# Kernel optimization log

Measured on AMD Instinct MI355X. Metric: run time of the kernel, lower is better.

The kernel has to match this reference:

```python
import jax, jax.numpy as jnp
import numpy as np

N, E, H, NODE_IN, EDGE_DIM, L = 10000, 400000, 128, 6, 3, 4
LN_EPS = 1e-5


def _lin_init(key, fan_in, fan_out):
    return jax.random.normal(key, (fan_in, fan_out), dtype=jnp.float32) / np.sqrt(fan_in)


def setup_inputs() -> dict:
    key = jax.random.key(0)
    ks = jax.random.split(key, 24)
    x = jax.random.normal(ks[0], (N, NODE_IN), dtype=jnp.float32)
    edge_index = jax.random.randint(ks[1], (2, E), 0, N, dtype=jnp.int64)
    edge_attr = jax.random.normal(ks[2], (E, EDGE_DIM), dtype=jnp.float32)
    # encoder
    enc_w1 = _lin_init(ks[3], NODE_IN, H); enc_b1 = jnp.zeros((H,), jnp.float32)
    enc_w2 = _lin_init(ks[4], H, H); enc_b2 = jnp.zeros((H,), jnp.float32)
    # per-layer stacked params [L, ...]
    msg_w1 = jax.vmap(lambda k: _lin_init(k, 2 * H + EDGE_DIM, H))(jax.random.split(ks[5], L))
    msg_b1 = jnp.zeros((L, H), jnp.float32)
    msg_w2 = jax.vmap(lambda k: _lin_init(k, H, H))(jax.random.split(ks[6], L))
    msg_b2 = jnp.zeros((L, H), jnp.float32)
    upd_w1 = jax.vmap(lambda k: _lin_init(k, 2 * H, H))(jax.random.split(ks[7], L))
    upd_b1 = jnp.zeros((L, H), jnp.float32)
    upd_w2 = jax.vmap(lambda k: _lin_init(k, H, H))(jax.random.split(ks[8], L))
    upd_b2 = jnp.zeros((L, H), jnp.float32)
    ln_g = jnp.ones((L, H), jnp.float32)
    ln_b = jnp.zeros((L, H), jnp.float32)
    # decoder
    dec_w1 = _lin_init(ks[9], H, H); dec_b1 = jnp.zeros((H,), jnp.float32)
    dec_w2 = _lin_init(ks[10], H, 1); dec_b2 = jnp.zeros((1,), jnp.float32)
    return dict(x=x, edge_index=edge_index, edge_attr=edge_attr,
                enc_w1=enc_w1, enc_b1=enc_b1, enc_w2=enc_w2, enc_b2=enc_b2,
                msg_w1=msg_w1, msg_b1=msg_b1, msg_w2=msg_w2, msg_b2=msg_b2,
                upd_w1=upd_w1, upd_b1=upd_b1, upd_w2=upd_w2, upd_b2=upd_b2,
                ln_g=ln_g, ln_b=ln_b,
                dec_w1=dec_w1, dec_b1=dec_b1, dec_w2=dec_w2, dec_b2=dec_b2)


def _layernorm(h, g, b):
    mu = jnp.mean(h, axis=-1, keepdims=True)
    var = jnp.mean(jnp.square(h - mu), axis=-1, keepdims=True)
    return (h - mu) * jax.lax.rsqrt(var + LN_EPS) * g + b


def reference(x, edge_index, edge_attr,
              enc_w1, enc_b1, enc_w2, enc_b2,
              msg_w1, msg_b1, msg_w2, msg_b2,
              upd_w1, upd_b1, upd_w2, upd_b2,
              ln_g, ln_b,
              dec_w1, dec_b1, dec_w2, dec_b2):
    src, tgt = edge_index[0], edge_index[1]  # PyG default flow: message from x_j=src to x_i=tgt
    # in-degree counts for mean aggregation (zero-degree nodes -> 0 output, like scatter_mean)
    counts = jax.ops.segment_sum(jnp.ones((E,), jnp.float32), tgt, num_segments=N)
    inv_counts = (1.0 / jnp.maximum(counts, 1.0))[:, None]
    # encoder
    h = jax.nn.relu(x @ enc_w1 + enc_b1) @ enc_w2 + enc_b2  # [N, H]
    for l in range(L):
        x_i = h[tgt]  # [E, H] target features
        x_j = h[src]  # [E, H] source features
        m_in = jnp.concatenate([x_i, x_j, edge_attr], axis=-1)  # [E, 2H+edge_dim]
        m = jax.nn.relu(m_in @ msg_w1[l] + msg_b1[l]) @ msg_w2[l] + msg_b2[l]  # [E, H]
        agg = jax.ops.segment_sum(m, tgt, num_segments=N) * inv_counts  # [N, H] mean aggregate
        u_in = jnp.concatenate([h, agg], axis=-1)  # [N, 2H]
        u = jax.nn.relu(u_in @ upd_w1[l] + upd_b1[l]) @ upd_w2[l] + upd_b2[l]
        h = _layernorm(u + h, ln_g[l], ln_b[l])  # residual (in==out channels)
    # decoder
    return jax.nn.relu(h @ dec_w1 + dec_b1) @ dec_w2 + dec_b2  # [N, 1]
```

## Files before the change

### kernel.cpp

```cpp
#include <hip/hip_runtime.h>

#define NN 10000
#define NE 400000
#define HD 128
#define NIN 6
#define EDIM 3
#define NL 4
#define CAP 96
#define LN_EPS 1e-5f

typedef unsigned short u16;
using short8 = __attribute__((ext_vector_type(8))) short;
using f32x4 = __attribute__((ext_vector_type(4))) float;

__device__ __forceinline__ u16 f2bf(float x) {
    unsigned u = __float_as_uint(x);
    return (u16)((u + 0x7fff + ((u >> 16) & 1)) >> 16);
}
__device__ __forceinline__ float bf2f(u16 h) { return __uint_as_float(((unsigned)h) << 16); }
__device__ __forceinline__ void split2(float x, u16& hi, u16& lo) {
    hi = f2bf(x);
    lo = f2bf(x - bf2f(hi));
}
#define MFMA(a, b, c) __builtin_amdgcn_mfma_f32_16x16x32_bf16((a), (b), (c), 0, 0, 0)


__global__ __launch_bounds__(256) void k_prep(const float* __restrict__ msg_w2, const float* __restrict__ msg_b2,
                                              const float* __restrict__ upd_w1, float* __restrict__ M2,
                                              float* __restrict__ c2, int* __restrict__ cnt) {
    int idx = blockIdx.x * 256 + threadIdx.x;
    if (idx < 65536) {
        int l = idx >> 14, rem = idx & 16383, i = rem >> 7, jj = rem & 127;
        const float* U1b = upd_w1 + (size_t)l * 2 * HD * HD + (size_t)HD * HD;
        const float* W2 = msg_w2 + (size_t)l * HD * HD + (size_t)i * HD;
        float acc = 0.f;
        for (int t = 0; t < HD; ++t) acc += W2[t] * U1b[(size_t)t * HD + jj];
        M2[idx] = acc;
    } else if (idx < 66048) {
        int r = idx - 65536;
        int l = r >> 7, jj = r & 127;
        const float* U1b = upd_w1 + (size_t)l * 2 * HD * HD + (size_t)HD * HD;
        const float* b2 = msg_b2 + l * HD;
        float acc = 0.f;
        for (int t = 0; t < HD; ++t) acc += b2[t] * U1b[(size_t)t * HD + jj];
        c2[r] = acc;
    } else if (idx < 76048) {
        cnt[idx - 66048] = 0;
    }
}


__global__ __launch_bounds__(256) void k_frag(const float* __restrict__ upd_w1, const float* __restrict__ M2,
                                              const float* __restrict__ upd_w2, const float* __restrict__ msg_w1,
                                              const float* __restrict__ dec_w1, const float* __restrict__ enc_w2,
                                              u16* __restrict__ fG1, u16* __restrict__ fG2, u16* __restrict__ fPQ,
                                              u16* __restrict__ fDec, u16* __restrict__ fEnc) {
    int g = blockIdx.x * 256 + threadIdx.x;
    if (g < 16384) {
        int l = g >> 12, r = g & 4095;
        int ct = r >> 9, ks = (r >> 6) & 7, lane = r & 63;
        int n = ct * 16 + (lane & 15), kb = ks * 32 + ((lane >> 4) << 3);
        u16* dst = fG1 + (size_t)g * 8;
        const float* U = upd_w1 + (size_t)l * 256 * 128;
        const float* Ml = M2 + (size_t)l * 128 * 128;
#pragma unroll
        for (int j = 0; j < 8; ++j) {
            int k = kb + j;
            float v = (k < 128) ? U[(size_t)k * 128 + n] : Ml[(size_t)(k - 128) * 128 + n];
            dst[j] = f2bf(v);
        }
    } else if (g < 24576) {
        int gg = g - 16384;
        int l = gg >> 11, r = gg & 2047;
        int ct = r >> 8, ks = (r >> 6) & 3, lane = r & 63;
        int n = ct * 16 + (lane & 15), kb = ks * 32 + ((lane >> 4) << 3);
        u16* dst = fG2 + (size_t)gg * 8;
        const float* W = upd_w2 + (size_t)l * 128 * 128;
#pragma unroll
        for (int j = 0; j < 8; ++j) dst[j] = f2bf(W[(size_t)(kb + j) * 128 + n]);
    } else if (g < 40960) {
        int gg = g - 24576;
        int li = gg >> 12, r = gg & 4095;
        int ct = r >> 8, ks = (r >> 6) & 3, lane = r & 63;
        int n = ct * 16 + (lane & 15), kb = ks * 32 + ((lane >> 4) << 3);
        u16* dst = fPQ + (size_t)gg * 8;
        const float* W = msg_w1 + (size_t)li * (2 * HD + EDIM) * HD;
#pragma unroll
        for (int j = 0; j < 8; ++j) {
            int k = kb + j;
            float v = (n < 128) ? W[(size_t)k * 128 + n] : W[(size_t)(128 + k) * 128 + (n - 128)];
            dst[j] = f2bf(v);
        }
    } else if (g < 43008) {
        int r = g - 40960;
        int ct = r >> 8, ks = (r >> 6) & 3, lane = r & 63;
        int n = ct * 16 + (lane & 15), kb = ks * 32 + ((lane >> 4) << 3);
        u16* dst = fDec + (size_t)r * 8;
#pragma unroll
        for (int j = 0; j < 8; ++j) dst[j] = f2bf(dec_w1[(size_t)(kb + j) * 128 + n]);
    } else if (g < 45056) {
        int r = g - 43008;
        int ct = r >> 8, ks = (r >> 6) & 3, lane = r & 63;
        int n = ct * 16 + (lane & 15), kb = ks * 32 + ((lane >> 4) << 3);
        u16* dst = fEnc + (size_t)r * 8;
#pragma unroll
        for (int j = 0; j < 8; ++j) dst[j] = f2bf(enc_w2[(size_t)(kb + j) * 128 + n]);
    }
}


__global__ __launch_bounds__(256) void k_scatter(const int* __restrict__ src, const int* __restrict__ tgt,
                                                 const float* __restrict__ ea, int* __restrict__ cnt,
                                                 float4* __restrict__ sea) {
    int e = blockIdx.x * 256 + threadIdx.x;
    if (e >= NE) return;
    int t = tgt[e];
    int pos = atomicAdd(&cnt[t], 1);
    if (pos < CAP) {
        sea[t * CAP + pos] =
            make_float4(ea[e * 3], ea[e * 3 + 1], ea[e * 3 + 2], __uint_as_float((unsigned)src[e]));
    }
}


__global__ __launch_bounds__(512) void k_enc(const float* __restrict__ x, const float* __restrict__ ew1,
                                             const float* __restrict__ eb1, const u16* __restrict__ fEnc,
                                             const float* __restrict__ eb2, const u16* __restrict__ fPQ0,
                                             const float* __restrict__ mb1, u16* __restrict__ h_hi,
                                             u16* __restrict__ h_lo, float* __restrict__ PQf,
                                             u16* __restrict__ Qb) {
    __shared__ u16 tHi[2048], tLo[2048];
    int tid = threadIdx.x, w = tid >> 6, lane = tid & 63, q = lane >> 4, c = lane & 15;
    int band = blockIdx.x * 16;
    {
        int col = w * 16 + c;
        float wv[NIN];
#pragma unroll
        for (int k = 0; k < NIN; ++k) wv[k] = ew1[k * HD + col];
        float ebv = eb1[col];
#pragma unroll
        for (int reg = 0; reg < 4; ++reg) {
            int row = band + q * 4 + reg;
            float t = ebv;
#pragma unroll
            for (int k = 0; k < NIN; ++k) t += x[(size_t)row * NIN + k] * wv[k];
            t = fmaxf(t, 0.f);
            u16 hi, lo;
            split2(t, hi, lo);
            int r16 = q * 4 + reg;
            int a = r16 * 128 + (((col >> 3) ^ r16) << 3) + (col & 7);
            tHi[a] = hi;
            tLo[a] = lo;
        }
    }
    __syncthreads();
    short8 aH[4], aL[4];
#pragma unroll
    for (int ks = 0; ks < 4; ++ks) {
        int a = c * 128 + (((ks * 4 + q) ^ c) << 3);
        aH[ks] = *(const short8*)&tHi[a];
        aL[ks] = *(const short8*)&tLo[a];
    }
    f32x4 acc = {0, 0, 0, 0};
    {
        const u16* fb = fEnc + (size_t)w * 4 * 512 + lane * 8;
#pragma unroll
        for (int ks = 0; ks < 4; ++ks) {
            short8 b = *(const short8*)(fb + ks * 512);
            acc = MFMA(aH[ks], b, acc);
            acc = MFMA(aL[ks], b, acc);
        }
    }
    __syncthreads();
    {
        int col = w * 16 + c;
        float ebv = eb2[col];
#pragma unroll
        for (int reg = 0; reg < 4; ++reg) {
            int r16 = q * 4 + reg, row = band + r16;
            float hval = acc[reg] + ebv;
            u16 hi, lo;
            split2(hval, hi, lo);
            h_hi[(size_t)row * HD + col] = hi;
            h_lo[(size_t)row * HD + col] = lo;
            int a = r16 * 128 + (((col >> 3) ^ r16) << 3) + (col & 7);
            tHi[a] = hi;
            tLo[a] = lo;
        }
    }
    __syncthreads();
#pragma unroll
    for (int ks = 0; ks < 4; ++ks) {
        int a = c * 128 + (((ks * 4 + q) ^ c) << 3);
        aH[ks] = *(const short8*)&tHi[a];
        aL[ks] = *(const short8*)&tLo[a];
    }
#pragma unroll
    for (int i = 0; i < 2; ++i) {
        int ctg = w * 2 + i;
        const u16* fb = fPQ0 + (size_t)ctg * 4 * 512 + lane * 8;
        f32x4 a3 = {0, 0, 0, 0};
#pragma unroll
        for (int ks = 0; ks < 4; ++ks) {
            short8 b = *(const short8*)(fb + ks * 512);
            a3 = MFMA(aH[ks], b, a3);
            a3 = MFMA(aL[ks], b, a3);
        }
        int col = ctg * 16 + c;
        if (ctg < 8) {
            float bias = mb1[col];
#pragma unroll
            for (int reg = 0; reg < 4; ++reg)
                PQf[(size_t)(band + q * 4 + reg) * HD + col] = a3[reg] + bias;
        } else {
            int colq = col - 128;
#pragma unroll
            for (int reg = 0; reg < 4; ++reg)
                Qb[(size_t)(band + q * 4 + reg) * HD + colq] = f2bf(a3[reg]);
        }
    }
}


template <bool LAST>
__global__ __launch_bounds__(512) void k_layer(
    const float* __restrict__ PQf_in, const u16* __restrict__ Qb_in,
    const int* __restrict__ cnt, const float4* __restrict__ sea, const float* __restrict__ wc,
    u16* __restrict__ h_hi, u16* __restrict__ h_lo,
    const u16* __restrict__ fG1, const u16* __restrict__ fG2,
    const float* __restrict__ ub1, const float* __restrict__ c2l, const float* __restrict__ ub2,
    const float* __restrict__ g, const float* __restrict__ bb,
    const u16* __restrict__ fPQ, const float* __restrict__ nb1,
    float* __restrict__ PQf_out, u16* __restrict__ Qb_out,
    const u16* __restrict__ fDec, const float* __restrict__ db1, const float* __restrict__ dw2,
    const float* __restrict__ db2, float* __restrict__ out) {
    __shared__ u16 sHi[2048], sLo[2048];
    __shared__ u16 tHi[2048], tLo[2048];
    __shared__ float red[16][8][2];
    int tid = threadIdx.x, w = tid >> 6, lane = tid & 63, q = lane >> 4, c = lane & 15;
    int band = blockIdx.x * 16;
    int j = lane * 2;
    {
        float2 wcr0 = *(const float2*)(wc + j);
        float2 wcr1 = *(const float2*)(wc + HD + j);
        float2 wcr2 = *(const float2*)(wc + 2 * HD + j);
#pragma unroll
        for (int i = 0; i < 2; ++i) {
            int r16 = w * 2 + i;
            int n = __builtin_amdgcn_readfirstlane(band + r16);
            int cn = cnt[n];
            float invn = 1.0f / fmaxf((float)cn, 1.0f);
            int cle = __builtin_amdgcn_readfirstlane(cn < CAP ? cn : CAP);
            float2 p = *(const float2*)(PQf_in + (size_t)n * HD + j);
            float acc0 = 0.f, acc1 = 0.f;
            const float4* bucket = sea + (size_t)n * CAP;
            auto edge1 = [&](float4 A) {
                int sv = (int)__float_as_uint(A.w);
                float c0 = A.x * wcr0.x + A.y * wcr1.x + A.z * wcr2.x;
                float c1 = A.x * wcr0.y + A.y * wcr1.y + A.z * wcr2.y;
                unsigned u = *(const unsigned*)(Qb_in + (size_t)sv * HD + j);
                acc0 += fmaxf(p.x + __uint_as_float(u << 16) + c0, 0.f);
                acc1 += fmaxf(p.y + __uint_as_float(u & 0xffff0000u) + c1, 0.f);
            };
            int e = 0;
            for (; e + 3 < cle; e += 4) {
                float4 A0 = bucket[e], A1 = bucket[e + 1], A2 = bucket[e + 2], A3 = bucket[e + 3];
                edge1(A0);
                edge1(A1);
                edge1(A2);
                edge1(A3);
            }
            for (; e < cle; ++e) edge1(bucket[e]);
            float v0 = acc0 * invn, v1 = acc1 * invn;
            u16 h0, l0, h1, l1;
            split2(v0, h0, l0);
            split2(v1, h1, l1);
            int a = r16 * 128 + (((j >> 3) ^ r16) << 3) + (j & 7);
            *(ushort2*)&sHi[a] = make_ushort2(h0, h1);
            *(ushort2*)&sLo[a] = make_ushort2(l0, l1);
        }
    }
    __syncthreads();
    short8 aH[8], aL[8];
    {
        size_t rb = (size_t)(band + c) * HD + q * 8;
#pragma unroll
        for (int ks = 0; ks < 4; ++ks) {
            aH[ks] = *(const short8*)(h_hi + rb + ks * 32);
            aL[ks] = *(const short8*)(h_lo + rb + ks * 32);
            int a = c * 128 + (((ks * 4 + q) ^ c) << 3);
            aH[4 + ks] = *(const short8*)&sHi[a];
            aL[4 + ks] = *(const short8*)&sLo[a];
        }
    }
    f32x4 acc = {0, 0, 0, 0};
    {
        const u16* fb = fG1 + (size_t)w * 8 * 512 + lane * 8;
#pragma unroll
        for (int ks = 0; ks < 8; ++ks) {
            short8 b = *(const short8*)(fb + ks * 512);
            acc = MFMA(aH[ks], b, acc);
            acc = MFMA(aL[ks], b, acc);
        }
    }
    float alv[4];
#pragma unroll
    for (int reg = 0; reg < 4; ++reg) alv[reg] = (cnt[band + q * 4 + reg] > 0) ? 1.f : 0.f;
    {
        int col = w * 16 + c;
        float u1b = ub1[col], cc = c2l[col];
#pragma unroll
        for (int reg = 0; reg < 4; ++reg) {
            int r16 = q * 4 + reg;
            float t = fmaxf(acc[reg] + u1b + alv[reg] * cc, 0.f);
            u16 hi, lo;
            split2(t, hi, lo);
            int a = r16 * 128 + (((col >> 3) ^ r16) << 3) + (col & 7);
            tHi[a] = hi;
            tLo[a] = lo;
        }
    }
    __syncthreads();
    short8 aH2[4], aL2[4];
#pragma unroll
    for (int ks = 0; ks < 4; ++ks) {
        int a = c * 128 + (((ks * 4 + q) ^ c) << 3);
        aH2[ks] = *(const short8*)&tHi[a];
        aL2[ks] = *(const short8*)&tLo[a];
    }
    f32x4 acc2 = {0, 0, 0, 0};
    {
        const u16* fb = fG2 + (size_t)w * 4 * 512 + lane * 8;
#pragma unroll
        for (int ks = 0; ks < 4; ++ks) {
            short8 b = *(const short8*)(fb + ks * 512);
            acc2 = MFMA(aH2[ks], b, acc2);
            acc2 = MFMA(aL2[ks], b, acc2);
        }
    }
    float vv[4];
    {
        int col = w * 16 + c;
        float u2b = ub2[col];
#pragma unroll
        for (int reg = 0; reg < 4; ++reg) {
            size_t idx = (size_t)(band + q * 4 + reg) * HD + col;
            float hres = bf2f(h_hi[idx]) + bf2f(h_lo[idx]);
            vv[reg] = acc2[reg] + u2b + hres;
        }
    }
#pragma unroll
    for (int reg = 0; reg < 4; ++reg) {
        float s = vv[reg];
        float s2 = vv[reg] * vv[reg];
        for (int m = 1; m < 16; m <<= 1) {
            s += __shfl_xor(s, m);
            s2 += __shfl_xor(s2, m);
        }
        if (c == 0) {
            red[q * 4 + reg][w][0] = s;
            red[q * 4 + reg][w][1] = s2;
        }
    }
    __syncthreads();
    float mu[4], rs[4];
#pragma unroll
    for (int reg = 0; reg < 4; ++reg) {
        int r16 = q * 4 + reg;
        float S1 = 0.f, S2 = 0.f;
#pragma unroll
        for (int ww = 0; ww < 8; ++ww) {
            S1 += red[r16][ww][0];
            S2 += red[r16][ww][1];
        }
        float m = S1 * (1.f / HD);
        float var = S2 * (1.f / HD) - m * m;
        mu[reg] = m;
        rs[reg] = rsqrtf(var + LN_EPS);
    }
    {
        int col = w * 16 + c;
        float gg = g[col], bv = bb[col];
#pragma unroll
        for (int reg = 0; reg < 4; ++reg) {
            int r16 = q * 4 + reg;
            float o = (vv[reg] - mu[reg]) * rs[reg] * gg + bv;
            u16 hi, lo;
            split2(o, hi, lo);
            int a = r16 * 128 + (((col >> 3) ^ r16) << 3) + (col & 7);
            tHi[a] = hi;
            tLo[a] = lo;
            if (!LAST) {
                size_t idx = (size_t)(band + r16) * HD + col;
                h_hi[idx] = hi;
                h_lo[idx] = lo;
            }
        }
    }
    __syncthreads();
    short8 aH3[4], aL3[4];
#pragma unroll
    for (int ks = 0; ks < 4; ++ks) {
        int a = c * 128 + (((ks * 4 + q) ^ c) << 3);
        aH3[ks] = *(const short8*)&tHi[a];
        aL3[ks] = *(const short8*)&tLo[a];
    }
    if (!LAST) {
#pragma unroll
        for (int i = 0; i < 2; ++i) {
            int ctg = w * 2 + i;
            const u16* fb = fPQ + (size_t)ctg * 4 * 512 + lane * 8;
            f32x4 a3 = {0, 0, 0, 0};
#pragma unroll
            for (int ks = 0; ks < 4; ++ks) {
                short8 b = *(const short8*)(fb + ks * 512);
                a3 = MFMA(aH3[ks], b, a3);
                a3 = MFMA(aL3[ks], b, a3);
            }
            int col = ctg * 16 + c;
            if (ctg < 8) {
                float bias = nb1[col];
#pragma unroll
                for (int reg = 0; reg < 4; ++reg)
                    PQf_out[(size_t)(band + q * 4 + reg) * HD + col] = a3[reg] + bias;
            } else {
                int colq = col - 128;
#pragma unroll
                for (int reg = 0; reg < 4; ++reg)
                    Qb_out[(size_t)(band + q * 4 + reg) * HD + colq] = f2bf(a3[reg]);
            }
        }
    } else {
        float part[4];
        {
            const u16* fb = fDec + (size_t)w * 4 * 512 + lane * 8;
            f32x4 a3 = {0, 0, 0, 0};
#pragma unroll
            for (int ks = 0; ks < 4; ++ks) {
                short8 b = *(const short8*)(fb + ks * 512);
                a3 = MFMA(aH3[ks], b, a3);
                a3 = MFMA(aL3[ks], b, a3);
            }
            int col = w * 16 + c;
            float w2v = dw2[col], b1v = db1[col];
#pragma unroll
            for (int reg = 0; reg < 4; ++reg) part[reg] = fmaxf(a3[reg] + b1v, 0.f) * w2v;
        }
#pragma unroll
        for (int reg = 0; reg < 4; ++reg) {
            float s = part[reg];
            for (int m = 1; m < 16; m <<= 1) s += __shfl_xor(s, m);
            if (c == 0) red[q * 4 + reg][w][0] = s;
        }
        __syncthreads();
        if (tid < 16) {
            float s = db2[0];
#pragma unroll
            for (int ww = 0; ww < 8; ++ww) s += red[tid][ww][0];
            out[band + tid] = s;
        }
    }
}


extern "C" void kernel_launch(void* const* d_in, const int* in_sizes, int n_in,
                              void* d_out, int out_size, void* d_ws, size_t ws_size,
                              hipStream_t stream) {
    const float* x = (const float*)d_in[0];
    const int* eidx = (const int*)d_in[1];
    const float* eattr = (const float*)d_in[2];
    const float* enc_w1 = (const float*)d_in[3];
    const float* enc_b1 = (const float*)d_in[4];
    const float* enc_w2 = (const float*)d_in[5];
    const float* enc_b2 = (const float*)d_in[6];
    const float* msg_w1 = (const float*)d_in[7];
    const float* msg_b1 = (const float*)d_in[8];
    const float* msg_w2 = (const float*)d_in[9];
    const float* msg_b2 = (const float*)d_in[10];
    const float* upd_w1 = (const float*)d_in[11];
    const float* upd_b1 = (const float*)d_in[12];
    const float* upd_w2 = (const float*)d_in[13];
    const float* upd_b2 = (const float*)d_in[14];
    const float* ln_g = (const float*)d_in[15];
    const float* ln_b = (const float*)d_in[16];
    const float* dec_w1 = (const float*)d_in[17];
    const float* dec_b1 = (const float*)d_in[18];
    const float* dec_w2 = (const float*)d_in[19];
    const float* dec_b2 = (const float*)d_in[20];
    const int* srcp = eidx;
    const int* tgtp = eidx + NE;

    char* base = (char*)d_ws;
    size_t off = 0;
    auto alloc = [&](size_t bytes) -> void* {
        off = (off + 15) & ~(size_t)15;
        void* p = base + off;
        off += bytes;
        return p;
    };
    float4* sea = (float4*)alloc((size_t)NN * CAP * 16);
    float* PQf0 = (float*)alloc((size_t)NN * HD * 4);
    float* PQf1 = (float*)alloc((size_t)NN * HD * 4);
    u16* Qb0 = (u16*)alloc((size_t)NN * HD * 2);
    u16* Qb1 = (u16*)alloc((size_t)NN * HD * 2);
    u16* h_hi = (u16*)alloc((size_t)NN * HD * 2);
    u16* h_lo = (u16*)alloc((size_t)NN * HD * 2);
    int* cnt = (int*)alloc((size_t)NN * 4);
    float* M2 = (float*)alloc((size_t)NL * HD * HD * 4);
    float* c2 = (float*)alloc((size_t)NL * HD * 4);
    u16* fG1 = (u16*)alloc((size_t)131072 * 2);
    u16* fG2 = (u16*)alloc((size_t)65536 * 2);
    u16* fPQ = (u16*)alloc((size_t)131072 * 2);
    u16* fDec = (u16*)alloc((size_t)16384 * 2);
    u16* fEnc = (u16*)alloc((size_t)16384 * 2);

    k_prep<<<298, 256, 0, stream>>>(msg_w2, msg_b2, upd_w1, M2, c2, cnt);
    k_frag<<<176, 256, 0, stream>>>(upd_w1, M2, upd_w2, msg_w1, dec_w1, enc_w2, fG1, fG2, fPQ, fDec, fEnc);
    k_scatter<<<(NE + 255) / 256, 256, 0, stream>>>(srcp, tgtp, eattr, cnt, sea);
    k_enc<<<NN / 16, 512, 0, stream>>>(x, enc_w1, enc_b1, fEnc, enc_b2, fPQ, msg_b1, h_hi, h_lo, PQf0, Qb0);

    float* PQin = PQf0;
    u16* Qin = Qb0;
    float* PQout = PQf1;
    u16* Qout = Qb1;
    for (int l = 0; l < NL; ++l) {
        const float* wc = msg_w1 + (size_t)l * (2 * HD + EDIM) * HD + (size_t)2 * HD * HD;
        if (l < NL - 1) {
            k_layer<false><<<NN / 16, 512, 0, stream>>>(
                PQin, Qin, cnt, sea, wc, h_hi, h_lo,
                fG1 + (size_t)l * 32768, fG2 + (size_t)l * 16384,
                upd_b1 + l * HD, c2 + l * HD, upd_b2 + l * HD, ln_g + l * HD, ln_b + l * HD,
                fPQ + (size_t)(l + 1) * 32768, msg_b1 + (size_t)(l + 1) * HD, PQout, Qout,
                nullptr, nullptr, nullptr, nullptr, nullptr);
        } else {
            k_layer<true><<<NN / 16, 512, 0, stream>>>(
                PQin, Qin, cnt, sea, wc, h_hi, h_lo,
                fG1 + (size_t)l * 32768, fG2 + (size_t)l * 16384,
                upd_b1 + l * HD, c2 + l * HD, upd_b2 + l * HD, ln_g + l * HD, ln_b + l * HD,
                nullptr, nullptr, nullptr, nullptr,
                fDec, dec_b1, dec_w2, dec_b2, (float*)d_out);
        }
        float* tf = PQin; PQin = PQout; PQout = tf;
        u16* tq = Qin; Qin = Qout; Qout = tq;
    }
}
```

Measured before the change: 286.5 us.

## Halve rows per layer block, merge prep/frag/scatter launches

```diff
diff --git a/kernel.cpp b/kernel.cpp
--- a/kernel.cpp
+++ b/kernel.cpp
@@ -25,9 +25,11 @@
 #define MFMA(a, b, c) __builtin_amdgcn_mfma_f32_16x16x32_bf16((a), (b), (c), 0, 0, 0)
 
 
-__global__ __launch_bounds__(256) void k_prep(const float* __restrict__ msg_w2, const float* __restrict__ msg_b2,
-                                              const float* __restrict__ upd_w1, float* __restrict__ M2,
-                                              float* __restrict__ c2, int* __restrict__ cnt) {
+__global__ __launch_bounds__(256) void k_prep(
+    const float* __restrict__ msg_w2, const float* __restrict__ msg_b2, const float* __restrict__ upd_w1,
+    const float* __restrict__ upd_w2, const float* __restrict__ msg_w1, const float* __restrict__ dec_w1,
+    const float* __restrict__ enc_w2, float* __restrict__ M2, float* __restrict__ c2, int* __restrict__ cnt,
+    u16* __restrict__ fG2, u16* __restrict__ fPQ, u16* __restrict__ fDec, u16* __restrict__ fEnc) {
     int idx = blockIdx.x * 256 + threadIdx.x;
     if (idx < 65536) {
         int l = idx >> 14, rem = idx & 16383, i = rem >> 7, jj = rem & 127;
@@ -46,17 +48,52 @@
         c2[r] = acc;
     } else if (idx < 76048) {
         cnt[idx - 66048] = 0;
-    }
-}
-
-
-__global__ __launch_bounds__(256) void k_frag(const float* __restrict__ upd_w1, const float* __restrict__ M2,
-                                              const float* __restrict__ upd_w2, const float* __restrict__ msg_w1,
-                                              const float* __restrict__ dec_w1, const float* __restrict__ enc_w2,
-                                              u16* __restrict__ fG1, u16* __restrict__ fG2, u16* __restrict__ fPQ,
-                                              u16* __restrict__ fDec, u16* __restrict__ fEnc) {
-    int g = blockIdx.x * 256 + threadIdx.x;
-    if (g < 16384) {
+    } else if (idx < 84240) {
+        int gg = idx - 76048;
+        int l = gg >> 11, r = gg & 2047;
+        int ct = r >> 8, ks = (r >> 6) & 3, lane = r & 63;
+        int n = ct * 16 + (lane & 15), kb = ks * 32 + ((lane >> 4) << 3);
+        u16* dst = fG2 + (size_t)gg * 8;
+        const float* W = upd_w2 + (size_t)l * 128 * 128;
+#pragma unroll
+        for (int j = 0; j < 8; ++j) dst[j] = f2bf(W[(size_t)(kb + j) * 128 + n]);
+    } else if (idx < 100624) {
+        int gg = idx - 84240;
+        int li = gg >> 12, r = gg & 4095;
+        int ct = r >> 8, ks = (r >> 6) & 3, lane = r & 63;
+        int n = ct * 16 + (lane & 15), kb = ks * 32 + ((lane >> 4) << 3);
+        u16* dst = fPQ + (size_t)gg * 8;
+        const float* W = msg_w1 + (size_t)li * (2 * HD + EDIM) * HD;
+#pragma unroll
+        for (int j = 0; j < 8; ++j) {
+            int k = kb + j;
+            float v = (n < 128) ? W[(size_t)k * 128 + n] : W[(size_t)(128 + k) * 128 + (n - 128)];
+            dst[j] = f2bf(v);
+        }
+    } else if (idx < 102672) {
+        int r = idx - 100624;
+        int ct = r >> 8, ks = (r >> 6) & 3, lane = r & 63;
+        int n = ct * 16 + (lane & 15), kb = ks * 32 + ((lane >> 4) << 3);
+        u16* dst = fDec + (size_t)r * 8;
+#pragma unroll
+        for (int j = 0; j < 8; ++j) dst[j] = f2bf(dec_w1[(size_t)(kb + j) * 128 + n]);
+    } else if (idx < 104720) {
+        int r = idx - 102672;
+        int ct = r >> 8, ks = (r >> 6) & 3, lane = r & 63;
+        int n = ct * 16 + (lane & 15), kb = ks * 32 + ((lane >> 4) << 3);
+        u16* dst = fEnc + (size_t)r * 8;
+#pragma unroll
+        for (int j = 0; j < 8; ++j) dst[j] = f2bf(enc_w2[(size_t)(kb + j) * 128 + n]);
+    }
+}
+
+
+__global__ __launch_bounds__(256) void k_scatfrag(
+    const int* __restrict__ src, const int* __restrict__ tgt, const float* __restrict__ ea,
+    int* __restrict__ cnt, float4* __restrict__ sea,
+    const float* __restrict__ upd_w1, const float* __restrict__ M2, u16* __restrict__ fG1) {
+    if (blockIdx.x < 64) {
+        int g = blockIdx.x * 256 + threadIdx.x;
         int l = g >> 12, r = g & 4095;
         int ct = r >> 9, ks = (r >> 6) & 7, lane = r & 63;
         int n = ct * 16 + (lane & 15), kb = ks * 32 + ((lane >> 4) << 3);
@@ -69,56 +106,15 @@
             float v = (k < 128) ? U[(size_t)k * 128 + n] : Ml[(size_t)(k - 128) * 128 + n];
             dst[j] = f2bf(v);
         }
-    } else if (g < 24576) {
-        int gg = g - 16384;
-        int l = gg >> 11, r = gg & 2047;
-        int ct = r >> 8, ks = (r >> 6) & 3, lane = r & 63;
-        int n = ct * 16 + (lane & 15), kb = ks * 32 + ((lane >> 4) << 3);
-        u16* dst = fG2 + (size_t)gg * 8;
-        const float* W = upd_w2 + (size_t)l * 128 * 128;
-#pragma unroll
-        for (int j = 0; j < 8; ++j) dst[j] = f2bf(W[(size_t)(kb + j) * 128 + n]);
-    } else if (g < 40960) {
-        int gg = g - 24576;
-        int li = gg >> 12, r = gg & 4095;
-        int ct = r >> 8, ks = (r >> 6) & 3, lane = r & 63;
-        int n = ct * 16 + (lane & 15), kb = ks * 32 + ((lane >> 4) << 3);
-        u16* dst = fPQ + (size_t)gg * 8;
-        const float* W = msg_w1 + (size_t)li * (2 * HD + EDIM) * HD;
-#pragma unroll
-        for (int j = 0; j < 8; ++j) {
-            int k = kb + j;
-            float v = (n < 128) ? W[(size_t)k * 128 + n] : W[(size_t)(128 + k) * 128 + (n - 128)];
-            dst[j] = f2bf(v);
-        }
-    } else if (g < 43008) {
-        int r = g - 40960;
-        int ct = r >> 8, ks = (r >> 6) & 3, lane = r & 63;
-        int n = ct * 16 + (lane & 15), kb = ks * 32 + ((lane >> 4) << 3);
-        u16* dst = fDec + (size_t)r * 8;
-#pragma unroll
-        for (int j = 0; j < 8; ++j) dst[j] = f2bf(dec_w1[(size_t)(kb + j) * 128 + n]);
-    } else if (g < 45056) {
-        int r = g - 43008;
-        int ct = r >> 8, ks = (r >> 6) & 3, lane = r & 63;
-        int n = ct * 16 + (lane & 15), kb = ks * 32 + ((lane >> 4) << 3);
-        u16* dst = fEnc + (size_t)r * 8;
-#pragma unroll
-        for (int j = 0; j < 8; ++j) dst[j] = f2bf(enc_w2[(size_t)(kb + j) * 128 + n]);
-    }
-}
-
-
-__global__ __launch_bounds__(256) void k_scatter(const int* __restrict__ src, const int* __restrict__ tgt,
-                                                 const float* __restrict__ ea, int* __restrict__ cnt,
-                                                 float4* __restrict__ sea) {
-    int e = blockIdx.x * 256 + threadIdx.x;
-    if (e >= NE) return;
-    int t = tgt[e];
-    int pos = atomicAdd(&cnt[t], 1);
-    if (pos < CAP) {
-        sea[t * CAP + pos] =
-            make_float4(ea[e * 3], ea[e * 3 + 1], ea[e * 3 + 2], __uint_as_float((unsigned)src[e]));
+    } else {
+        int e = (blockIdx.x - 64) * 256 + threadIdx.x;
+        if (e >= NE) return;
+        int t = tgt[e];
+        int pos = atomicAdd(&cnt[t], 1);
+        if (pos < CAP) {
+            sea[t * CAP + pos] =
+                make_float4(ea[e * 3], ea[e * 3 + 1], ea[e * 3 + 2], __uint_as_float((unsigned)src[e]));
+        }
     }
 }
 
@@ -236,76 +232,72 @@
     const float* __restrict__ db2, float* __restrict__ out) {
     __shared__ u16 sHi[2048], sLo[2048];
     __shared__ u16 tHi[2048], tLo[2048];
-    __shared__ float red[16][8][2];
+    __shared__ float red[8][8][2];
     int tid = threadIdx.x, w = tid >> 6, lane = tid & 63, q = lane >> 4, c = lane & 15;
-    int band = blockIdx.x * 16;
+    int band = blockIdx.x * 8;
     int j = lane * 2;
     {
         float2 wcr0 = *(const float2*)(wc + j);
         float2 wcr1 = *(const float2*)(wc + HD + j);
         float2 wcr2 = *(const float2*)(wc + 2 * HD + j);
-#pragma unroll
-        for (int i = 0; i < 2; ++i) {
-            int r16 = w * 2 + i;
-            int n = __builtin_amdgcn_readfirstlane(band + r16);
-            int cn = cnt[n];
-            float invn = 1.0f / fmaxf((float)cn, 1.0f);
-            int cle = __builtin_amdgcn_readfirstlane(cn < CAP ? cn : CAP);
-            float2 p = *(const float2*)(PQf_in + (size_t)n * HD + j);
-            float acc0 = 0.f, acc1 = 0.f;
-            const float4* bucket = sea + (size_t)n * CAP;
-            auto edge1 = [&](float4 A) {
-                int sv = (int)__float_as_uint(A.w);
-                float c0 = A.x * wcr0.x + A.y * wcr1.x + A.z * wcr2.x;
-                float c1 = A.x * wcr0.y + A.y * wcr1.y + A.z * wcr2.y;
-                unsigned u = *(const unsigned*)(Qb_in + (size_t)sv * HD + j);
-                acc0 += fmaxf(p.x + __uint_as_float(u << 16) + c0, 0.f);
-                acc1 += fmaxf(p.y + __uint_as_float(u & 0xffff0000u) + c1, 0.f);
-            };
-            int e = 0;
-            for (; e + 3 < cle; e += 4) {
-                float4 A0 = bucket[e], A1 = bucket[e + 1], A2 = bucket[e + 2], A3 = bucket[e + 3];
-                edge1(A0);
-                edge1(A1);
-                edge1(A2);
-                edge1(A3);
-            }
-            for (; e < cle; ++e) edge1(bucket[e]);
-            float v0 = acc0 * invn, v1 = acc1 * invn;
-            u16 h0, l0, h1, l1;
-            split2(v0, h0, l0);
-            split2(v1, h1, l1);
-            int a = r16 * 128 + (((j >> 3) ^ r16) << 3) + (j & 7);
-            *(ushort2*)&sHi[a] = make_ushort2(h0, h1);
-            *(ushort2*)&sLo[a] = make_ushort2(l0, l1);
-        }
-    }
-    __syncthreads();
-    short8 aH[8], aL[8];
-    {
+        int n = __builtin_amdgcn_readfirstlane(band + w);
+        int cn = cnt[n];
+        float invn = 1.0f / fmaxf((float)cn, 1.0f);
+        int cle = __builtin_amdgcn_readfirstlane(cn < CAP ? cn : CAP);
+        float2 p = *(const float2*)(PQf_in + (size_t)n * HD + j);
+        float acc0 = 0.f, acc1 = 0.f;
+        const float4* bucket = sea + (size_t)n * CAP;
+        auto edge1 = [&](float4 A) {
+            int sv = (int)__float_as_uint(A.w);
+            float c0 = A.x * wcr0.x + A.y * wcr1.x + A.z * wcr2.x;
+            float c1 = A.x * wcr0.y + A.y * wcr1.y + A.z * wcr2.y;
+            unsigned u = *(const unsigned*)(Qb_in + (size_t)sv * HD + j);
+            acc0 += fmaxf(p.x + __uint_as_float(u << 16) + c0, 0.f);
+            acc1 += fmaxf(p.y + __uint_as_float(u & 0xffff0000u) + c1, 0.f);
+        };
+        int e = 0;
+        for (; e + 3 < cle; e += 4) {
+            float4 A0 = bucket[e], A1 = bucket[e + 1], A2 = bucket[e + 2], A3 = bucket[e + 3];
+            edge1(A0);
+            edge1(A1);
+            edge1(A2);
+            edge1(A3);
+        }
+        for (; e < cle; ++e) edge1(bucket[e]);
+        float v0 = acc0 * invn, v1 = acc1 * invn;
+        u16 h0, l0, h1, l1;
+        split2(v0, h0, l0);
+        split2(v1, h1, l1);
+        int a = w * 128 + (((j >> 3) ^ w) << 3) + (j & 7);
+        *(ushort2*)&sHi[a] = make_ushort2(h0, h1);
+        *(ushort2*)&sLo[a] = make_ushort2(l0, l1);
+    }
+    __syncthreads();
+    f32x4 acc = {0, 0, 0, 0};
+    {
+        const u16* fb = fG1 + (size_t)w * 8 * 512 + lane * 8;
         size_t rb = (size_t)(band + c) * HD + q * 8;
 #pragma unroll
         for (int ks = 0; ks < 4; ++ks) {
-            aH[ks] = *(const short8*)(h_hi + rb + ks * 32);
-            aL[ks] = *(const short8*)(h_lo + rb + ks * 32);
+            short8 aH = *(const short8*)(h_hi + rb + ks * 32);
+            short8 aL = *(const short8*)(h_lo + rb + ks * 32);
+            short8 b = *(const short8*)(fb + ks * 512);
+            acc = MFMA(aH, b, acc);
+            acc = MFMA(aL, b, acc);
+        }
+#pragma unroll
+        for (int ks = 0; ks < 4; ++ks) {
             int a = c * 128 + (((ks * 4 + q) ^ c) << 3);
-            aH[4 + ks] = *(const short8*)&sHi[a];
-            aL[4 + ks] = *(const short8*)&sLo[a];
-        }
-    }
-    f32x4 acc = {0, 0, 0, 0};
-    {
-        const u16* fb = fG1 + (size_t)w * 8 * 512 + lane * 8;
-#pragma unroll
-        for (int ks = 0; ks < 8; ++ks) {
-            short8 b = *(const short8*)(fb + ks * 512);
-            acc = MFMA(aH[ks], b, acc);
-            acc = MFMA(aL[ks], b, acc);
+            short8 aH = *(const short8*)&sHi[a];
+            short8 aL = *(const short8*)&sLo[a];
+            short8 b = *(const short8*)(fb + (4 + ks) * 512);
+            acc = MFMA(aH, b, acc);
+            acc = MFMA(aL, b, acc);
         }
     }
     float alv[4];
 #pragma unroll
-    for (int reg = 0; reg < 4; ++reg) alv[reg] = (cnt[band + q * 4 + reg] > 0) ? 1.f : 0.f;
+    for (int reg = 0; reg < 4; ++reg) alv[reg] = (cnt[band + ((q * 4 + reg) & 7)] > 0) ? 1.f : 0.f;
     {
         int col = w * 16 + c;
         float u1b = ub1[col], cc = c2l[col];
@@ -321,21 +313,17 @@
         }
     }
     __syncthreads();
-    short8 aH2[4], aL2[4];
-#pragma unroll
-    for (int ks = 0; ks < 4; ++ks) {
-        int a = c * 128 + (((ks * 4 + q) ^ c) << 3);
-        aH2[ks] = *(const short8*)&tHi[a];
-        aL2[ks] = *(const short8*)&tLo[a];
-    }
     f32x4 acc2 = {0, 0, 0, 0};
     {
         const u16* fb = fG2 + (size_t)w * 4 * 512 + lane * 8;
 #pragma unroll
         for (int ks = 0; ks < 4; ++ks) {
+            int a = c * 128 + (((ks * 4 + q) ^ c) << 3);
+            short8 aH = *(const short8*)&tHi[a];
+            short8 aL = *(const short8*)&tLo[a];
             short8 b = *(const short8*)(fb + ks * 512);
-            acc2 = MFMA(aH2[ks], b, acc2);
-            acc2 = MFMA(aL2[ks], b, acc2);
+            acc2 = MFMA(aH, b, acc2);
+            acc2 = MFMA(aL, b, acc2);
         }
     }
     float vv[4];
@@ -344,7 +332,8 @@
         float u2b = ub2[col];
 #pragma unroll
         for (int reg = 0; reg < 4; ++reg) {
-            size_t idx = (size_t)(band + q * 4 + reg) * HD + col;
+            int r16 = q * 4 + reg;
+            size_t idx = (size_t)(band + (r16 & 7)) * HD + col;
             float hres = bf2f(h_hi[idx]) + bf2f(h_lo[idx]);
             vv[reg] = acc2[reg] + u2b + hres;
         }
@@ -357,9 +346,10 @@
             s += __shfl_xor(s, m);
             s2 += __shfl_xor(s2, m);
         }
-        if (c == 0) {
-            red[q * 4 + reg][w][0] = s;
-            red[q * 4 + reg][w][1] = s2;
+        int r16 = q * 4 + reg;
+        if (c == 0 && r16 < 8) {
+            red[r16][w][0] = s;
+            red[r16][w][1] = s2;
         }
     }
     __syncthreads();
@@ -367,16 +357,21 @@
 #pragma unroll
     for (int reg = 0; reg < 4; ++reg) {
         int r16 = q * 4 + reg;
-        float S1 = 0.f, S2 = 0.f;
-#pragma unroll
-        for (int ww = 0; ww < 8; ++ww) {
-            S1 += red[r16][ww][0];
-            S2 += red[r16][ww][1];
-        }
-        float m = S1 * (1.f / HD);
-        float var = S2 * (1.f / HD) - m * m;
-        mu[reg] = m;
-        rs[reg] = rsqrtf(var + LN_EPS);
+        if (r16 < 8) {
+            float S1 = 0.f, S2 = 0.f;
+#pragma unroll
+            for (int ww = 0; ww < 8; ++ww) {
+                S1 += red[r16][ww][0];
+                S2 += red[r16][ww][1];
+            }
+            float m = S1 * (1.f / HD);
+            float var = S2 * (1.f / HD) - m * m;
+            mu[reg] = m;
+            rs[reg] = rsqrtf(var + LN_EPS);
+        } else {
+            mu[reg] = 0.f;
+            rs[reg] = 1.f;
+        }
     }
     {
         int col = w * 16 + c;
@@ -390,7 +385,7 @@
             int a = r16 * 128 + (((col >> 3) ^ r16) << 3) + (col & 7);
             tHi[a] = hi;
             tLo[a] = lo;
-            if (!LAST) {
+            if (!LAST && r16 < 8) {
                 size_t idx = (size_t)(band + r16) * HD + col;
                 h_hi[idx] = hi;
                 h_lo[idx] = lo;
@@ -421,13 +416,17 @@
             if (ctg < 8) {
                 float bias = nb1[col];
 #pragma unroll
-                for (int reg = 0; reg < 4; ++reg)
-                    PQf_out[(size_t)(band + q * 4 + reg) * HD + col] = a3[reg] + bias;
+                for (int reg = 0; reg < 4; ++reg) {
+                    int r16 = q * 4 + reg;
+                    if (r16 < 8) PQf_out[(size_t)(band + r16) * HD + col] = a3[reg] + bias;
+                }
             } else {
                 int colq = col - 128;
 #pragma unroll
-                for (int reg = 0; reg < 4; ++reg)
-                    Qb_out[(size_t)(band + q * 4 + reg) * HD + colq] = f2bf(a3[reg]);
+                for (int reg = 0; reg < 4; ++reg) {
+                    int r16 = q * 4 + reg;
+                    if (r16 < 8) Qb_out[(size_t)(band + r16) * HD + colq] = f2bf(a3[reg]);
+                }
             }
         }
     } else {
@@ -450,10 +449,11 @@
         for (int reg = 0; reg < 4; ++reg) {
             float s = part[reg];
             for (int m = 1; m < 16; m <<= 1) s += __shfl_xor(s, m);
-            if (c == 0) red[q * 4 + reg][w][0] = s;
+            int r16 = q * 4 + reg;
+            if (c == 0 && r16 < 8) red[r16][w][0] = s;
         }
         __syncthreads();
-        if (tid < 16) {
+        if (tid < 8) {
             float s = db2[0];
 #pragma unroll
             for (int ww = 0; ww < 8; ++ww) s += red[tid][ww][0];
@@ -514,9 +514,9 @@
     u16* fDec = (u16*)alloc((size_t)16384 * 2);
     u16* fEnc = (u16*)alloc((size_t)16384 * 2);
 
-    k_prep<<<298, 256, 0, stream>>>(msg_w2, msg_b2, upd_w1, M2, c2, cnt);
-    k_frag<<<176, 256, 0, stream>>>(upd_w1, M2, upd_w2, msg_w1, dec_w1, enc_w2, fG1, fG2, fPQ, fDec, fEnc);
-    k_scatter<<<(NE + 255) / 256, 256, 0, stream>>>(srcp, tgtp, eattr, cnt, sea);
+    k_prep<<<410, 256, 0, stream>>>(msg_w2, msg_b2, upd_w1, upd_w2, msg_w1, dec_w1, enc_w2,
+                                    M2, c2, cnt, fG2, fPQ, fDec, fEnc);
+    k_scatfrag<<<64 + (NE + 255) / 256, 256, 0, stream>>>(srcp, tgtp, eattr, cnt, sea, upd_w1, M2, fG1);
     k_enc<<<NN / 16, 512, 0, stream>>>(x, enc_w1, enc_b1, fEnc, enc_b2, fPQ, msg_b1, h_hi, h_lo, PQf0, Qb0);
 
     float* PQin = PQf0;
@@ -526,14 +526,14 @@
     for (int l = 0; l < NL; ++l) {
         const float* wc = msg_w1 + (size_t)l * (2 * HD + EDIM) * HD + (size_t)2 * HD * HD;
         if (l < NL - 1) {
-            k_layer<false><<<NN / 16, 512, 0, stream>>>(
+            k_layer<false><<<NN / 8, 512, 0, stream>>>(
                 PQin, Qin, cnt, sea, wc, h_hi, h_lo,
                 fG1 + (size_t)l * 32768, fG2 + (size_t)l * 16384,
                 upd_b1 + l * HD, c2 + l * HD, upd_b2 + l * HD, ln_g + l * HD, ln_b + l * HD,
                 fPQ + (size_t)(l + 1) * 32768, msg_b1 + (size_t)(l + 1) * HD, PQout, Qout,
                 nullptr, nullptr, nullptr, nullptr, nullptr);
         } else {
-            k_layer<true><<<NN / 16, 512, 0, stream>>>(
+            k_layer<true><<<NN / 8, 512, 0, stream>>>(
                 PQin, Qin, cnt, sea, wc, h_hi, h_lo,
                 fG1 + (size_t)l * 32768, fG2 + (size_t)l * 16384,
                 upd_b1 + l * HD, c2 + l * HD, upd_b2 + l * HD, ln_g + l * HD, ln_b + l * HD,
```

Result: slower. 310.7 us (+8.5%).
